# Kernel tuning notes

Measured on AMD Instinct MI355X. Metric: run time of the kernel, lower is better.

Reference implementation:

```python
import jax, jax.numpy as jnp
from jax import lax
import numpy as np

B, H, W = 8, 96, 96
CIN, COUT, QD, NH = 256, 128, 32, 8
LA_MID = COUT // 8  # 16
GRIDS = (6, 3, 2, 1)
EPS = 1e-5  # torch BatchNorm default eps


def conv2d(x, w):
    # 'same' padding for 3x3 stride 1 (autopad k//2)
    return lax.conv_general_dilated(x, w, (1, 1), 'SAME',
                                    dimension_numbers=('NCHW', 'OIHW', 'NCHW'))


def bn2d(x, g, b, m, v):
    inv = g / jnp.sqrt(v + EPS)
    return x * inv[None, :, None, None] + (b - m * inv)[None, :, None, None]


def adaptive_avg_pool_tokens(x, oh, ow):
    # matches torch adaptive_avg_pool2d bin edges; returns [b, c, oh*ow]
    b, c, h, w = x.shape
    cells = []
    for i in range(oh):
        h0, h1 = (i * h) // oh, -((-(i + 1) * h) // oh)
        for j in range(ow):
            w0, w1 = (j * w) // ow, -((-(j + 1) * w) // ow)
            cells.append(x[:, :, h0:h1, w0:w1].mean(axis=(2, 3)))
    return jnp.stack(cells, axis=-1)


def psp(x, grids):
    b, c, h, w = x.shape
    ar = w / h
    return jnp.concatenate(
        [adaptive_avg_pool_tokens(x, g, max(1, round(ar * g))) for g in grids], axis=2)


def setup_inputs() -> dict:
    key = jax.random.key(0)
    ks = jax.random.split(key, 9)
    f = jnp.float32
    return {
        'x': jax.random.normal(ks[0], (B, CIN, H, W), f),
        'w_red': jax.random.normal(ks[1], (COUT, CIN, 3, 3), f) * 0.02,
        'bng': jnp.ones((COUT,), f), 'bnb': jnp.zeros((COUT,), f),
        'bnm': jnp.zeros((COUT,), f), 'bnv': jnp.ones((COUT,), f),
        'w_q': jax.random.normal(ks[2], (QD, COUT), f) * 0.1,
        'b_q': jnp.zeros((QD,), f),
        'w_k': jax.random.normal(ks[3], (QD, COUT), f) * 0.1,
        'b_k': jnp.zeros((QD,), f),
        'w_v': jax.random.normal(ks[4], (COUT, COUT), f) * 0.08,
        'b_v': jnp.zeros((COUT,), f),
        'lsh': jax.random.normal(ks[5], (NH, QD), f),
        'w_la1': jax.random.normal(ks[6], (LA_MID, COUT), f) * 0.1,
        'lag': jnp.ones((LA_MID,), f), 'lab': jnp.zeros((LA_MID,), f),
        'lam': jnp.zeros((LA_MID,), f), 'lav': jnp.ones((LA_MID,), f),
        'w_la2': jax.random.normal(ks[7], (COUT, LA_MID, 3, 3), f) * 0.02,
    }


def reference(x, w_red, bng, bnb, bnm, bnv, w_q, b_q, w_k, b_k, w_v, b_v,
              lsh, w_la1, lag, lab, lam, lav, w_la2):
    # reduce_channel: Conv(256,128,3) = conv + BN + SiLU
    xr = jax.nn.silu(bn2d(conv2d(x, w_red), bng, bnb, bnm, bnv))  # [B,COUT,H,W]
    b, c, h, w = xr.shape
    # query: 1x1 conv to 32 ch, flatten spatial -> [B, HW, QD]
    q = (jnp.einsum('oc,bchw->bohw', w_q, xr)
         + b_q[None, :, None, None]).reshape(b, QD, h * w).transpose(0, 2, 1)
    # key_psp and value_psp act on the same xr -> identical token sets [B,COUT,50]
    tokens = psp(xr, GRIDS)
    k_tok = (jnp.einsum('oc,bcn->bon', w_k, tokens)
             + b_k[None, :, None]).transpose(0, 2, 1)  # [B,50,QD]
    v_tok = (jnp.einsum('oc,bcn->bon', w_v, tokens)
             + b_v[None, :, None]).transpose(0, 2, 1)  # [B,50,COUT]
    # ReformerAttention: argmax over TOKEN dim -> [B, NH]; sort indices lie in [0,NH)
    # so the gather picks a per-batch permutation of the first NH key/value tokens
    # (faithful to the torch code; q_buckets is computed but unused there).
    k_buckets = jnp.argmax(jnp.einsum('hd,bnd->bhn', lsh, k_tok), axis=-1)  # [B,NH]
    k_idx = jnp.argsort(k_buckets, axis=-1)  # [B,NH], values in [0,NH)
    k_s = jnp.take_along_axis(k_tok, k_idx[:, :, None], axis=1)  # [B,NH,QD]
    v_s = jnp.take_along_axis(v_tok, k_idx[:, :, None], axis=1)  # [B,NH,COUT]
    att = jax.nn.softmax(jnp.einsum('bqd,bkd->bqk', q, k_s), axis=-1)  # [B,HW,NH]
    ctx = jnp.einsum('bqk,bkd->bqd', att, v_s).transpose(0, 2, 1).reshape(b, COUT, h, w)
    # LocalAttenModule: Conv(128,16,1)(conv+bn+silu) -> 3x3 conv 16->128 -> tanh mask
    y = jax.nn.silu(bn2d(jnp.einsum('oc,bchw->bohw', w_la1, ctx), lag, lab, lam, lav))
    mask = jnp.tanh(conv2d(y, w_la2))
    ctx = ctx * mask + ctx
    return xr + ctx
```

## Files before the change

### kernel.cpp

```cpp
#include <hip/hip_runtime.h>
#include <hip/hip_bf16.h>
#include <cmath>

typedef __attribute__((ext_vector_type(8))) short short8;
typedef __attribute__((ext_vector_type(16))) short short16;
typedef __attribute__((ext_vector_type(4))) short s16x4;
typedef __attribute__((ext_vector_type(4))) float f32x4;
typedef __attribute__((ext_vector_type(2))) float f32x2;
typedef unsigned short u16;

#define HW 9216

__device__ inline float bf2f(u16 u) {
    union { unsigned int i; float f; } x; x.i = ((unsigned int)u) << 16; return x.f;
}
__device__ inline u16 f2bf(float f) {
    union { unsigned int i; float f; } x; x.f = f;
    unsigned int r = x.i + 0x7FFF + ((x.i >> 16) & 1);
    return (u16)(r >> 16);
}

__device__ inline void gload16(const u16* g, u16* l) {
    __builtin_amdgcn_global_load_lds(
        (const __attribute__((address_space(1))) void*)g,
        (__attribute__((address_space(3))) void*)l,
        16, 0, 0);
}

__global__ __launch_bounds__(256) void transform_w(
    const float* __restrict__ wred, const float* __restrict__ wla2,
    u16* __restrict__ Wt1, u16* __restrict__ Wt2)
{
    int idx = blockIdx.x * 256 + threadIdx.x;
    if (idx < 128 * 2304) {
        int co = idx / 2304;
        int rem = idx - co * 2304;
        int c = rem / 288;
        int r2 = rem - c * 288;
        int khw = r2 >> 5, ciL = r2 & 31;
        Wt1[idx] = f2bf(wred[((co * 256 + c * 32 + ciL) * 9 + khw)]);
    } else {
        int i2 = idx - 128 * 2304;
        if (i2 < 128 * 160) {
            int co = i2 / 160;
            int k = i2 - co * 160;
            int khw = k >> 4, ci = k & 15;
            Wt2[i2] = (khw < 9) ? f2bf(wla2[((co << 4) + ci) * 9 + khw]) : (u16)0;
        }
    }
}

__global__ __launch_bounds__(256) void transpose_x(
    const float* __restrict__ X, u16* __restrict__ Xt)
{
    __shared__ u16 Lt[256][66];
    int t = threadIdx.x;
    int bid = blockIdx.x;
    int b = bid & 7;
    int p0 = (bid >> 3) * 64;
    int pp = t & 63, c4 = t >> 6;
    const float* xb = X + (size_t)b * 256 * HW + p0 + pp;
    for (int r = 0; r < 64; ++r) {
        int c = r * 4 + c4;
        Lt[c][pp] = f2bf(xb[(size_t)c * HW]);
    }
    __syncthreads();
    int p = t >> 2, cq = t & 3;
    u16* ot = Xt + ((size_t)b * HW + p0 + p) * 256 + cq * 64;
#pragma unroll
    for (int o = 0; o < 4; ++o) {
        short16 v;
#pragma unroll
        for (int j = 0; j < 16; ++j)
            v[j] = (short)Lt[cq * 64 + o * 16 + j][p];
        *(short16*)(ot + o * 16) = v;
    }
}

template<int CIN, int KTILES, int KP, int EPI>
__global__ __launch_bounds__(256) void conv_k(
    const u16* __restrict__ Xt, const u16* __restrict__ Wt,
    u16* OutH, float* OutF,
    const float* __restrict__ bg, const float* __restrict__ bb,
    const float* __restrict__ bm, const float* __restrict__ bv,
    const u16* __restrict__ xrb, const float* ctxf,
    const u16* __restrict__ zp)
{
    __shared__ __align__(16) short As[2][128 * 32];
    __shared__ __align__(16) short Bs[2][96 * 32];
    __shared__ float invA[128], betA[128];

    const int tid = threadIdx.x;
    const int bid = blockIdx.x;
    const int b = bid & 7;
    const int tile = bid >> 3;
    const int w0 = (tile % 3) * 32;
    const int h0 = (tile / 3) * 3;

    const int lane = tid & 63;
    const int wid = tid >> 6;
    const int wm = (wid & 1) * 64;
    const int wn = (wid >> 1) * 48;
    const int r = lane & 15;
    const int quad = lane >> 4;

    if constexpr (EPI == 1) {
        if (tid < 128) {
            float iv = bg[tid] * rsqrtf(bv[tid] + 1e-5f);
            invA[tid] = iv;
            betA[tid] = bb[tid] - bm[tid] * iv;
        }
    }

    const u16* XtB = Xt + (size_t)b * HW * CIN;

    auto bsrc = [&](int slot, int kt) -> const u16* {
        int row = slot >> 2, o = slot & 3;
        int pw = row & 31, ph = row >> 5;
        int hgl = h0 + ph, wgl = w0 + pw;
        if (CIN == 256) {
            int c = (kt * 57) >> 9;
            int khw = kt - c * 9;
            int dh = (khw * 11) >> 5;
            int dw = khw - 3 * dh;
            int hh = hgl + dh - 1, ww = wgl + dw - 1;
            bool ok = ((unsigned)hh < 96u) && ((unsigned)ww < 96u);
            return ok ? XtB + ((size_t)hh * 96 + ww) * 256 + c * 32 + o * 8 : zp;
        } else {
            int kg = kt * 32 + o * 8;
            int khw = kg >> 4, ci0 = kg & 15;
            int dh = (khw * 11) >> 5, dw = khw - 3 * dh;
            int hh = hgl + dh - 1, ww = wgl + dw - 1;
            bool ok = ((unsigned)hh < 96u) && ((unsigned)ww < 96u) && (khw < 9);
            return ok ? XtB + ((size_t)hh * 96 + ww) * 16 + ci0 : zp;
        }
    };

    auto stage = [&](int kt, int buf) {
        int sA0 = tid, sA1 = tid + 256;
        gload16(Wt + (size_t)(sA0 >> 2) * KP + kt * 32 + (sA0 & 3) * 8,
                (u16*)&As[buf][(64 * wid) * 8]);
        gload16(Wt + (size_t)(sA1 >> 2) * KP + kt * 32 + (sA1 & 3) * 8,
                (u16*)&As[buf][(256 + 64 * wid) * 8]);
        gload16(bsrc(tid, kt), (u16*)&Bs[buf][(64 * wid) * 8]);
        if (wid < 2)
            gload16(bsrc(tid + 256, kt), (u16*)&Bs[buf][(256 + 64 * wid) * 8]);
    };

    f32x4 acc[4][3];
    f32x4 zz = {0.f, 0.f, 0.f, 0.f};
#pragma unroll
    for (int i = 0; i < 4; i++)
#pragma unroll
        for (int j = 0; j < 3; j++) acc[i][j] = zz;

    stage(0, 0);
    __syncthreads();

    for (int kt = 0; kt < KTILES; ++kt) {
        int cur = kt & 1;
        if (kt + 1 < KTILES) stage(kt + 1, cur ^ 1);
        short8 af[4], bfr[3];
#pragma unroll
        for (int i = 0; i < 4; i++)
            af[i] = *(const short8*)(&As[cur][(wm + i * 16 + r) * 32 + quad * 8]);
#pragma unroll
        for (int j = 0; j < 3; j++)
            bfr[j] = *(const short8*)(&Bs[cur][(wn + j * 16 + r) * 32 + quad * 8]);
        __builtin_amdgcn_s_setprio(1);
#pragma unroll
        for (int i = 0; i < 4; i++)
#pragma unroll
            for (int j = 0; j < 3; j++)
                acc[i][j] = __builtin_amdgcn_mfma_f32_16x16x32_bf16(af[i], bfr[j], acc[i][j], 0, 0, 0);
        __builtin_amdgcn_s_setprio(0);
        if (kt + 1 < KTILES)
            __syncthreads();
    }

#pragma unroll
    for (int i = 0; i < 4; i++) {
#pragma unroll
        for (int j = 0; j < 3; j++) {
            int pl = wn + j * 16 + r;
            int w = w0 + (pl & 31), h = h0 + (pl >> 5);
#pragma unroll
            for (int g = 0; g < 4; ++g) {
                int co = wm + i * 16 + quad * 4 + g;
                float v = acc[i][j][g];
                size_t oidx = ((size_t)b * 128 + co) * HW + h * 96 + w;
                if constexpr (EPI == 1) {
                    float val = v * invA[co] + betA[co];
                    float sv = val / (1.f + __expf(-val));
                    OutH[oidx] = f2bf(sv);
                } else {
                    float xv = bf2f(xrb[oidx]);
                    float cv = ctxf[oidx];
                    float e = __expf(2.f * v);
                    float th = 1.f - 2.f / (e + 1.f);
                    OutF[oidx] = xv + cv * (1.f + th);
                }
            }
        }
    }
}

__global__ __launch_bounds__(256) void prep_attn(
    const u16* __restrict__ xr,
    const float* __restrict__ wk, const float* __restrict__ bk,
    const float* __restrict__ wv, const float* __restrict__ bv,
    const float* __restrict__ wq, const float* __restrict__ bq,
    const float* __restrict__ wla1,
    float* __restrict__ Aout, float* __restrict__ Vout, float* __restrict__ c0out,
    float* __restrict__ WVout)
{
    __shared__ float part[256];
    __shared__ float tok[128];
    __shared__ float ks[32];
    __shared__ float vs[128];
    int t = threadIdx.x;
    int bid = blockIdx.x;
    int b = bid & 7, n = bid >> 3;
    int c = t & 127, half = t >> 7;
    int i0 = (n < 6) ? 0 : 16;
    int j0 = ((n < 6) ? n : (n - 6)) * 16;
    const u16* xb = xr + (size_t)(b * 128 + c) * HW;

    float s = 0.f;
    for (int rr = 0; rr < 8; ++rr) {
        int row = i0 + half * 8 + rr;
        const u16* rp = xb + row * 96 + j0;
        short8 v0 = *(const short8*)rp;
        short8 v1 = *(const short8*)(rp + 8);
#pragma unroll
        for (int j = 0; j < 8; ++j) s += bf2f((u16)v0[j]) + bf2f((u16)v1[j]);
    }
    part[t] = s;
    __syncthreads();
    if (t < 128) tok[t] = (part[t] + part[t + 128]) * (1.f / 256.f);
    __syncthreads();
    if (t < 32) {
        float s2 = bk[t];
        for (int cc = 0; cc < 128; ++cc) s2 += wk[t * 128 + cc] * tok[cc];
        ks[t] = s2;
    }
    __syncthreads();
    if (t < 128) {
        float s3 = bv[c];
        for (int c2 = 0; c2 < 128; ++c2) s3 += wv[c * 128 + c2] * tok[c2];
        Vout[((size_t)b * 8 + n) * 128 + c] = s3;
        vs[c] = s3;
    } else {
        float s4 = 0.f;
        for (int d = 0; d < 32; ++d) s4 += wq[d * 128 + c] * ks[d];
        Aout[((size_t)b * 8 + n) * 128 + c] = s4;
    }
    if (t == 0) {
        float s5 = 0.f;
        for (int d = 0; d < 32; ++d) s5 += bq[d] * ks[d];
        c0out[b * 8 + n] = s5;
    }
    __syncthreads();
    if (t < 16) {
        float s6 = 0.f;
        for (int cc = 0; cc < 128; ++cc) s6 += vs[cc] * wla1[t * 128 + cc];
        WVout[((size_t)b * 8 + n) * 16 + t] = s6;
    }
}

__global__ __launch_bounds__(256) void attn_k(
    const u16* __restrict__ xr,
    const float* __restrict__ Ain, const float* __restrict__ Vin,
    const float* __restrict__ c0in, const float* __restrict__ WVin,
    const float* __restrict__ lag, const float* __restrict__ lab,
    const float* __restrict__ lam, const float* __restrict__ lav,
    float* __restrict__ ctxout, u16* __restrict__ yout)
{
    __shared__ __align__(16) u16 Xh[128 * 64];
    __shared__ __align__(16) float Ast[128 * 8];
    __shared__ __align__(16) float Vst[128 * 8];
    __shared__ float WVs[128];
    __shared__ float satt[8 * 64];
    __shared__ float c0s[8], inv1[16], bet1[16];

    int t = threadIdx.x;
    int bid = blockIdx.x;
    int b = bid & 7;
    int p0 = (bid >> 3) * 64;

    for (int i = t; i < 1024; i += 256) {
        int n = i >> 7, c = i & 127;
        Ast[c * 8 + n] = Ain[b * 1024 + i];
        Vst[c * 8 + n] = Vin[b * 1024 + i];
    }
    if (t < 128) WVs[t] = WVin[b * 128 + t];
    if (t < 8) c0s[t] = c0in[b * 8 + t];
    if (t < 16) {
        float iv = lag[t] * rsqrtf(lav[t] + 1e-5f);
        inv1[t] = iv; bet1[t] = lab[t] - lam[t] * iv;
    }
    const u16* xb = xr + (size_t)b * 128 * HW + p0;
#pragma unroll
    for (int it = 0; it < 4; ++it) {
        int c = (t >> 3) + it * 32;
        int seg = t & 7;
        short8 v = *(const short8*)(xb + (size_t)c * HW + seg * 8);
        *(short8*)(&Xh[c * 64 + seg * 8]) = v;
    }
    __syncthreads();
    {
        int pp = t & 63, ng = t >> 6;
        float a0 = 0.f, a1 = 0.f;
        for (int c = 0; c < 128; ++c) {
            float x = bf2f(Xh[c * 64 + pp]);
            f32x2 av = *(const f32x2*)(&Ast[c * 8 + ng * 2]);
            a0 += av[0] * x;
            a1 += av[1] * x;
        }
        satt[(ng * 2) * 64 + pp] = a0 + c0s[ng * 2];
        satt[(ng * 2 + 1) * 64 + pp] = a1 + c0s[ng * 2 + 1];
    }
    __syncthreads();
    if (t < 64) {
        float m = -1e30f;
        float sv[8];
#pragma unroll
        for (int n = 0; n < 8; ++n) { sv[n] = satt[n * 64 + t]; m = fmaxf(m, sv[n]); }
        float sum = 0.f;
#pragma unroll
        for (int n = 0; n < 8; ++n) { sv[n] = __expf(sv[n] - m); sum += sv[n]; }
        float rcp = 1.f / sum;
#pragma unroll
        for (int n = 0; n < 8; ++n) satt[n * 64 + t] = sv[n] * rcp;
    }
    __syncthreads();
    {
        int pp = t & 63, cg = t >> 6;
        float at[8];
#pragma unroll
        for (int n = 0; n < 8; ++n) at[n] = satt[n * 64 + pp];
        for (int ci = 0; ci < 32; ++ci) {
            int c = cg * 32 + ci;
            f32x4 v0 = *(const f32x4*)(&Vst[c * 8]);
            f32x4 v1 = *(const f32x4*)(&Vst[c * 8 + 4]);
            float s = at[0] * v0[0] + at[1] * v0[1] + at[2] * v0[2] + at[3] * v0[3]
                    + at[4] * v1[0] + at[5] * v1[1] + at[6] * v1[2] + at[7] * v1[3];
            ctxout[((size_t)b * 128 + c) * HW + p0 + pp] = s;
        }
        float a[4] = {0.f, 0.f, 0.f, 0.f};
#pragma unroll
        for (int n = 0; n < 8; ++n) {
            f32x4 wv = *(const f32x4*)(&WVs[n * 16 + cg * 4]);
#pragma unroll
            for (int k = 0; k < 4; ++k) a[k] += at[n] * wv[k];
        }
        s16x4 pk;
#pragma unroll
        for (int k = 0; k < 4; ++k) {
            int d = cg * 4 + k;
            float val = a[k] * inv1[d] + bet1[d];
            float s = val / (1.f + __expf(-val));
            pk[k] = (short)f2bf(s);
        }
        *(s16x4*)(yout + ((size_t)b * HW + p0 + pp) * 16 + cg * 4) = pk;
    }
}

extern "C" void kernel_launch(void* const* d_in, const int* in_sizes, int n_in,
                              void* d_out, int out_size, void* d_ws, size_t ws_size,
                              hipStream_t stream)
{
    const float* x    = (const float*)d_in[0];
    const float* wred = (const float*)d_in[1];
    const float* bng  = (const float*)d_in[2];
    const float* bnb  = (const float*)d_in[3];
    const float* bnm  = (const float*)d_in[4];
    const float* bnv  = (const float*)d_in[5];
    const float* wq   = (const float*)d_in[6];
    const float* bq   = (const float*)d_in[7];
    const float* wk   = (const float*)d_in[8];
    const float* bk   = (const float*)d_in[9];
    const float* wv   = (const float*)d_in[10];
    const float* bv   = (const float*)d_in[11];
    const float* wla1 = (const float*)d_in[13];
    const float* lag  = (const float*)d_in[14];
    const float* lab  = (const float*)d_in[15];
    const float* lam  = (const float*)d_in[16];
    const float* lav  = (const float*)d_in[17];
    const float* wla2 = (const float*)d_in[18];

    char* ws = (char*)d_ws;
    u16*   xr  = (u16*)(ws + 0);
    u16*   yt  = (u16*)(ws + 18874368);
    u16*   Wt1 = (u16*)(ws + 21233664);
    u16*   Wt2 = (u16*)(ws + 21823488);
    float* Ab  = (float*)(ws + 21864448);
    float* Vb  = (float*)(ws + 21897216);
    float* c0b = (float*)(ws + 21929984);
    float* WVb = (float*)(ws + 21930240);
    u16*   xt   = (u16*)d_out;
    float* outp = (float*)d_out;
    const u16* zp = Wt2 + 144;

    transform_w<<<dim3(1232), dim3(256), 0, stream>>>(wred, wla2, Wt1, Wt2);

    transpose_x<<<dim3(1152), dim3(256), 0, stream>>>(x, xt);

    conv_k<256, 72, 2304, 1><<<dim3(768), dim3(256), 0, stream>>>(
        xt, Wt1, xr, nullptr, bng, bnb, bnm, bnv, nullptr, nullptr, zp);

    prep_attn<<<dim3(64), dim3(256), 0, stream>>>(
        xr, wk, bk, wv, bv, wq, bq, wla1, Ab, Vb, c0b, WVb);

    attn_k<<<dim3(1152), dim3(256), 0, stream>>>(
        xr, Ab, Vb, c0b, WVb, lag, lab, lam, lav, outp, yt);

    conv_k<16, 5, 160, 2><<<dim3(768), dim3(256), 0, stream>>>(
        yt, Wt2, nullptr, outp, nullptr, nullptr, nullptr, nullptr, xr, outp, zp);
}
```

Measured before the change: 279.2 us.

## Triple-buffer conv loads, merge prep kernels, and re-layout attention LDS

New measurement: 276.1 us. No clear change (-1.1%).

```diff
diff --git a/kernel.cpp b/kernel.cpp
--- a/kernel.cpp
+++ b/kernel.cpp
@@ -27,53 +27,56 @@
         16, 0, 0);
 }
 
-__global__ __launch_bounds__(256) void transform_w(
+#define VWAIT4 asm volatile("s_waitcnt vmcnt(4)" ::: "memory")
+#define VWAIT3 asm volatile("s_waitcnt vmcnt(3)" ::: "memory")
+#define VWAIT0 asm volatile("s_waitcnt vmcnt(0)" ::: "memory")
+
+__global__ __launch_bounds__(256) void prex_k(
+    const float* __restrict__ X, u16* __restrict__ Xt,
     const float* __restrict__ wred, const float* __restrict__ wla2,
     u16* __restrict__ Wt1, u16* __restrict__ Wt2)
 {
-    int idx = blockIdx.x * 256 + threadIdx.x;
-    if (idx < 128 * 2304) {
-        int co = idx / 2304;
-        int rem = idx - co * 2304;
-        int c = rem / 288;
-        int r2 = rem - c * 288;
-        int khw = r2 >> 5, ciL = r2 & 31;
-        Wt1[idx] = f2bf(wred[((co * 256 + c * 32 + ciL) * 9 + khw)]);
-    } else {
-        int i2 = idx - 128 * 2304;
-        if (i2 < 128 * 160) {
-            int co = i2 / 160;
-            int k = i2 - co * 160;
-            int khw = k >> 4, ci = k & 15;
-            Wt2[i2] = (khw < 9) ? f2bf(wla2[((co << 4) + ci) * 9 + khw]) : (u16)0;
-        }
-    }
-}
-
-__global__ __launch_bounds__(256) void transpose_x(
-    const float* __restrict__ X, u16* __restrict__ Xt)
-{
-    __shared__ u16 Lt[256][66];
+    __shared__ u16 Lt[256 * 35];
     int t = threadIdx.x;
     int bid = blockIdx.x;
-    int b = bid & 7;
-    int p0 = (bid >> 3) * 64;
-    int pp = t & 63, c4 = t >> 6;
-    const float* xb = X + (size_t)b * 256 * HW + p0 + pp;
-    for (int r = 0; r < 64; ++r) {
-        int c = r * 4 + c4;
-        Lt[c][pp] = f2bf(xb[(size_t)c * HW]);
-    }
-    __syncthreads();
-    int p = t >> 2, cq = t & 3;
-    u16* ot = Xt + ((size_t)b * HW + p0 + p) * 256 + cq * 64;
-#pragma unroll
-    for (int o = 0; o < 4; ++o) {
-        short16 v;
-#pragma unroll
-        for (int j = 0; j < 16; ++j)
-            v[j] = (short)Lt[cq * 64 + o * 16 + j][p];
-        *(short16*)(ot + o * 16) = v;
+    if (bid < 2304) {
+        int b = bid & 7;
+        int p0 = (bid >> 3) * 32;
+        int pp = t & 31, cg = t >> 5;
+        const float* xb = X + (size_t)b * 256 * HW + p0 + pp;
+        for (int r = 0; r < 32; ++r) {
+            int c = r * 8 + cg;
+            Lt[c * 35 + pp] = f2bf(xb[(size_t)c * HW]);
+        }
+        __syncthreads();
+        int p = t >> 3, cq = t & 7;
+        u16* ot = Xt + ((size_t)b * HW + p0 + p) * 256 + cq * 32;
+#pragma unroll
+        for (int o = 0; o < 2; ++o) {
+            short16 v;
+#pragma unroll
+            for (int j = 0; j < 16; ++j)
+                v[j] = (short)Lt[(cq * 32 + o * 16 + j) * 35 + p];
+            *(short16*)(ot + o * 16) = v;
+        }
+    } else {
+        int idx = (bid - 2304) * 256 + t;
+        if (idx < 128 * 2304) {
+            int co = idx / 2304;
+            int rem = idx - co * 2304;
+            int c = rem / 288;
+            int r2 = rem - c * 288;
+            int khw = r2 >> 5, ciL = r2 & 31;
+            Wt1[idx] = f2bf(wred[((co * 256 + c * 32 + ciL) * 9 + khw)]);
+        } else {
+            int i2 = idx - 128 * 2304;
+            if (i2 < 128 * 160) {
+                int co = i2 / 160;
+                int k = i2 - co * 160;
+                int khw = k >> 4, ci = k & 15;
+                Wt2[i2] = (khw < 9) ? f2bf(wla2[((co << 4) + ci) * 9 + khw]) : (u16)0;
+            }
+        }
     }
 }
 
@@ -86,8 +89,8 @@
     const u16* __restrict__ xrb, const float* ctxf,
     const u16* __restrict__ zp)
 {
-    __shared__ __align__(16) short As[2][128 * 32];
-    __shared__ __align__(16) short Bs[2][96 * 32];
+    __shared__ __align__(16) short As[3][128 * 32];
+    __shared__ __align__(16) short Bs[3][96 * 32];
     __shared__ float invA[128], betA[128];
 
     const int tid = threadIdx.x;
@@ -103,14 +106,6 @@
     const int wn = (wid >> 1) * 48;
     const int r = lane & 15;
     const int quad = lane >> 4;
-
-    if constexpr (EPI == 1) {
-        if (tid < 128) {
-            float iv = bg[tid] * rsqrtf(bv[tid] + 1e-5f);
-            invA[tid] = iv;
-            betA[tid] = bb[tid] - bm[tid] * iv;
-        }
-    }
 
     const u16* XtB = Xt + (size_t)b * HW * CIN;
 
@@ -155,11 +150,13 @@
         for (int j = 0; j < 3; j++) acc[i][j] = zz;
 
     stage(0, 0);
-    __syncthreads();
+    stage(1, 1);
+    if (wid < 2) VWAIT4; else VWAIT3;
+    __builtin_amdgcn_s_barrier();
 
     for (int kt = 0; kt < KTILES; ++kt) {
-        int cur = kt & 1;
-        if (kt + 1 < KTILES) stage(kt + 1, cur ^ 1);
+        int cur = kt % 3;
+        if (kt + 2 < KTILES) stage(kt + 2, (kt + 2) % 3);
         short8 af[4], bfr[3];
 #pragma unroll
         for (int i = 0; i < 4; i++)
@@ -174,8 +171,20 @@
             for (int j = 0; j < 3; j++)
                 acc[i][j] = __builtin_amdgcn_mfma_f32_16x16x32_bf16(af[i], bfr[j], acc[i][j], 0, 0, 0);
         __builtin_amdgcn_s_setprio(0);
-        if (kt + 1 < KTILES)
-            __syncthreads();
+        if (kt + 1 < KTILES) {
+            if (kt + 2 < KTILES) { if (wid < 2) VWAIT4; else VWAIT3; }
+            else VWAIT0;
+            __builtin_amdgcn_s_barrier();
+        }
+    }
+
+    if constexpr (EPI == 1) {
+        if (tid < 128) {
+            float iv = bg[tid] * rsqrtf(bv[tid] + 1e-5f);
+            invA[tid] = iv;
+            betA[tid] = bb[tid] - bm[tid] * iv;
+        }
+        __syncthreads();
     }
 
 #pragma unroll
@@ -276,9 +285,9 @@
     const float* __restrict__ lam, const float* __restrict__ lav,
     float* __restrict__ ctxout, u16* __restrict__ yout)
 {
-    __shared__ __align__(16) u16 Xh[128 * 64];
-    __shared__ __align__(16) float Ast[128 * 8];
-    __shared__ __align__(16) float Vst[128 * 8];
+    __shared__ __align__(16) u16 Xh[64 * 136];
+    __shared__ __align__(16) float Ast[8 * 128];
+    __shared__ __align__(16) float Vst[8 * 128];
     __shared__ float WVs[128];
     __shared__ float satt[8 * 64];
     __shared__ float c0s[8], inv1[16], bet1[16];
@@ -289,9 +298,8 @@
     int p0 = (bid >> 3) * 64;
 
     for (int i = t; i < 1024; i += 256) {
-        int n = i >> 7, c = i & 127;
-        Ast[c * 8 + n] = Ain[b * 1024 + i];
-        Vst[c * 8 + n] = Vin[b * 1024 + i];
+        Ast[i] = Ain[b * 1024 + i];
+        Vst[i] = Vin[b * 1024 + i];
     }
     if (t < 128) WVs[t] = WVin[b * 128 + t];
     if (t < 8) c0s[t] = c0in[b * 8 + t];
@@ -305,17 +313,33 @@
         int c = (t >> 3) + it * 32;
         int seg = t & 7;
         short8 v = *(const short8*)(xb + (size_t)c * HW + seg * 8);
-        *(short8*)(&Xh[c * 64 + seg * 8]) = v;
+#pragma unroll
+        for (int j = 0; j < 8; ++j)
+            Xh[(seg * 8 + j) * 136 + c] = (u16)v[j];
     }
     __syncthreads();
     {
         int pp = t & 63, ng = t >> 6;
+        const float* A0 = &Ast[(ng * 2) * 128];
+        const float* A1 = &Ast[(ng * 2 + 1) * 128];
+        const u16* xrow = &Xh[pp * 136];
         float a0 = 0.f, a1 = 0.f;
-        for (int c = 0; c < 128; ++c) {
-            float x = bf2f(Xh[c * 64 + pp]);
-            f32x2 av = *(const f32x2*)(&Ast[c * 8 + ng * 2]);
-            a0 += av[0] * x;
-            a1 += av[1] * x;
+        for (int c8 = 0; c8 < 16; ++c8) {
+            short8 xv = *(const short8*)(&xrow[c8 * 8]);
+            f32x4 q00 = *(const f32x4*)(&A0[c8 * 8]);
+            f32x4 q01 = *(const f32x4*)(&A0[c8 * 8 + 4]);
+            f32x4 q10 = *(const f32x4*)(&A1[c8 * 8]);
+            f32x4 q11 = *(const f32x4*)(&A1[c8 * 8 + 4]);
+#pragma unroll
+            for (int j = 0; j < 4; ++j) {
+                float x = bf2f((u16)xv[j]);
+                a0 += q00[j] * x; a1 += q10[j] * x;
+            }
+#pragma unroll
+            for (int j = 0; j < 4; ++j) {
+                float x = bf2f((u16)xv[j + 4]);
+                a0 += q01[j] * x; a1 += q11[j] * x;
+            }
         }
         satt[(ng * 2) * 64 + pp] = a0 + c0s[ng * 2];
         satt[(ng * 2 + 1) * 64 + pp] = a1 + c0s[ng * 2 + 1];
@@ -339,13 +363,20 @@
         float at[8];
 #pragma unroll
         for (int n = 0; n < 8; ++n) at[n] = satt[n * 64 + pp];
-        for (int ci = 0; ci < 32; ++ci) {
-            int c = cg * 32 + ci;
-            f32x4 v0 = *(const f32x4*)(&Vst[c * 8]);
-            f32x4 v1 = *(const f32x4*)(&Vst[c * 8 + 4]);
-            float s = at[0] * v0[0] + at[1] * v0[1] + at[2] * v0[2] + at[3] * v0[3]
-                    + at[4] * v1[0] + at[5] * v1[1] + at[6] * v1[2] + at[7] * v1[3];
-            ctxout[((size_t)b * 128 + c) * HW + p0 + pp] = s;
+        for (int c4 = 0; c4 < 8; ++c4) {
+            int c = cg * 32 + c4 * 4;
+            float s0 = 0.f, s1 = 0.f, s2 = 0.f, s3 = 0.f;
+#pragma unroll
+            for (int n = 0; n < 8; ++n) {
+                f32x4 vv = *(const f32x4*)(&Vst[n * 128 + c]);
+                s0 += at[n] * vv[0]; s1 += at[n] * vv[1];
+                s2 += at[n] * vv[2]; s3 += at[n] * vv[3];
+            }
+            size_t obase = ((size_t)b * 128 + c) * HW + p0 + pp;
+            ctxout[obase] = s0;
+            ctxout[obase + HW] = s1;
+            ctxout[obase + 2 * HW] = s2;
+            ctxout[obase + 3 * HW] = s3;
         }
         float a[4] = {0.f, 0.f, 0.f, 0.f};
 #pragma unroll
@@ -402,9 +433,7 @@
     float* outp = (float*)d_out;
     const u16* zp = Wt2 + 144;
 
-    transform_w<<<dim3(1232), dim3(256), 0, stream>>>(wred, wla2, Wt1, Wt2);
-
-    transpose_x<<<dim3(1152), dim3(256), 0, stream>>>(x, xt);
+    prex_k<<<dim3(3536), dim3(256), 0, stream>>>(x, xt, wred, wla2, Wt1, Wt2);
 
     conv_k<256, 72, 2304, 1><<<dim3(768), dim3(256), 0, stream>>>(
         xt, Wt1, xr, nullptr, bng, bnb, bnm, bnv, nullptr, nullptr, zp);
```
